# Kernel tuning notes

Measured on AMD Instinct MI355X. Metric: run time of the kernel, lower is better.

## Reference

```python
import jax, jax.numpy as jnp
import numpy as np

B, N, H = 16, 1024, 1024


def setup_inputs() -> dict:
    key = jax.random.key(0)
    ks = jax.random.split(key, 12)
    inv = 1.0 / np.sqrt(H)
    inp = {
        "x": jax.random.normal(ks[0], (B, N, H), jnp.float32),
        "atom_graph": jax.random.normal(ks[1], (B, N, N), jnp.float32),
        "variable_graph": jax.random.normal(ks[2], (B, N, N), jnp.float32),
        "Wq": jax.random.uniform(ks[3], (H, H), jnp.float32, -inv, inv),
        "bq": jax.random.uniform(ks[4], (H,), jnp.float32, -inv, inv),
        "Wk": jax.random.uniform(ks[5], (H, H), jnp.float32, -inv, inv),
        "bk": jax.random.uniform(ks[6], (H,), jnp.float32, -inv, inv),
        "Wv": jax.random.uniform(ks[7], (H, H), jnp.float32, -inv, inv),
        "bv": jax.random.uniform(ks[8], (H,), jnp.float32, -inv, inv),
        "predicate_pos": jax.random.randint(ks[9], (B, N), 0, 2, jnp.int32),
        "variable_tags": jax.random.randint(ks[10], (B, N), 0, 4, jnp.int32),
    }
    return inp


def _path_pool(h, predicate_pos):
    # h: [B,N,H]; predicate_pos: [B,N] in {0,1}
    b, n, d = h.shape
    i = jnp.arange(n)
    # pos[i-2] (value irrelevant for i<2, those branches handled explicitly)
    pp2 = jnp.pad(predicate_pos, ((0, 0), (2, 0)))[:, :n]  # [B,N]
    # window [s, e): i==0 -> [0,2); i==1 -> [0,3); pos[i-2]==1 -> [i,i+2); else [i-1,i+2)
    s = jnp.where(i < 2, 0, jnp.where(pp2 == 1, i, i - 1))  # [B,N]
    e = jnp.where(i == 0, 2, jnp.where(i == 1, 3, i + 2))    # [N]
    e = jnp.minimum(e, n)
    e = jnp.broadcast_to(e, (b, n))
    # prefix sums along node dim with a leading zero row -> windowed means via gather
    cs = jnp.concatenate([jnp.zeros((b, 1, d), h.dtype), jnp.cumsum(h, axis=1)], axis=1)  # [B,N+1,H]
    win_sum = (jnp.take_along_axis(cs, e[:, :, None], axis=1)
               - jnp.take_along_axis(cs, s[:, :, None], axis=1))  # [B,N,H]
    means = win_sum / (e - s)[:, :, None].astype(h.dtype)
    mask = (predicate_pos == 1).astype(h.dtype)  # [B,N]
    item = (means * mask[:, :, None]).sum(axis=1) / mask.sum(axis=1)[:, None]  # [B,H]
    return jnp.broadcast_to(item[:, None, :], (b, n, d))


def reference(x, atom_graph, variable_graph, Wq, bq, Wk, bk, Wv, bv,
              predicate_pos, variable_tags):
    scale = x.shape[-1] ** (-0.5)
    q = (x @ Wq.T + bq) * scale
    k = x @ Wk.T + bk
    v = x @ Wv.T + bv
    att = jnp.einsum("bnh,bmh->bnm", q, k) + atom_graph + variable_graph
    att = jax.nn.softmax(att, axis=-1)  # dropout is identity in eval
    h = jnp.einsum("bnm,bmh->bnh", att, v)
    return _path_pool(h, predicate_pos)
```

## Files before the change

kernel.cpp:

```cpp
#include <hip/hip_runtime.h>
#include <hip/hip_bf16.h>

#define BATCH 16
#define SEQ   1024
#define DIM   1024

typedef __attribute__((ext_vector_type(8))) short bf16x8;
typedef __attribute__((ext_vector_type(4))) float f32x4;
typedef __attribute__((ext_vector_type(4))) unsigned short us4;

__device__ __forceinline__ float bfu2f(unsigned short u) {
  union { unsigned int i; float f; } c; c.i = ((unsigned int)u) << 16; return c.f;
}
__device__ __forceinline__ unsigned short f2bfu(float f) {
  union { float f; unsigned int i; } c; c.f = f;
  return (unsigned short)((c.i + 0x7FFFu + ((c.i >> 16) & 1u)) >> 16);
}
__device__ __forceinline__ void async16(void* lds, const void* g) {
  __builtin_amdgcn_global_load_lds(
      (const __attribute__((address_space(1))) unsigned int*)g,
      (__attribute__((address_space(3))) unsigned int*)lds, 16, 0, 0);
}

__global__ void cast_xw_kernel(const float* __restrict__ x, const float* __restrict__ Wv,
                               unsigned short* __restrict__ xb,
                               unsigned short* __restrict__ Wvb, int x4) {
  int i = blockIdx.x * blockDim.x + threadIdx.x;
  const float* in; unsigned short* out; int j;
  if (i < x4) { in = x; out = xb; j = i; }
  else { in = Wv; out = Wvb; j = i - x4; }
  f32x4 v = ((const f32x4*)in)[j];
  us4 o;
  o[0] = f2bfu(v[0]); o[1] = f2bfu(v[1]); o[2] = f2bfu(v[2]); o[3] = f2bfu(v[3]);
  ((us4*)out)[j] = o;
}

__global__ void castT_kernel(const float* __restrict__ Wq, const float* __restrict__ Wk,
                             unsigned short* __restrict__ WqT,
                             unsigned short* __restrict__ WkT) {
  const float* in = (blockIdx.z == 0) ? Wq : Wk;
  unsigned short* out = (blockIdx.z == 0) ? WqT : WkT;
  __shared__ float t[64][65];
  const int h0 = blockIdx.x * 64, i0 = blockIdx.y * 64;
  const int tid = threadIdx.x;
  const int sub = tid >> 4, c4 = tid & 15;
#pragma unroll
  for (int p = 0; p < 4; ++p) {
    const int row = p * 16 + sub;
    f32x4 v = *(const f32x4*)(in + (size_t)(h0 + row) * DIM + i0 + c4 * 4);
    t[row][c4 * 4 + 0] = v[0]; t[row][c4 * 4 + 1] = v[1];
    t[row][c4 * 4 + 2] = v[2]; t[row][c4 * 4 + 3] = v[3];
  }
  __syncthreads();
#pragma unroll
  for (int p = 0; p < 4; ++p) {
    const int orow = p * 16 + sub;
    us4 o;
    o[0] = f2bfu(t[c4 * 4 + 0][orow]);
    o[1] = f2bfu(t[c4 * 4 + 1][orow]);
    o[2] = f2bfu(t[c4 * 4 + 2][orow]);
    o[3] = f2bfu(t[c4 * 4 + 3][orow]);
    *(us4*)(out + (size_t)(i0 + orow) * DIM + h0 + c4 * 4) = o;
  }
}

__global__ void t12_kernel(const unsigned short* __restrict__ WqT,
                           const unsigned short* __restrict__ WkT,
                           const float* __restrict__ bq, const float* __restrict__ bk,
                           float* __restrict__ t1, float* __restrict__ t2) {
  const int y = blockIdx.y;
  const unsigned short* Wt = y ? WkT : WqT;
  const float* vec = y ? bq : bk;
  float* tout = y ? t2 : t1;
  const int wave = threadIdx.x >> 6, lane = threadIdx.x & 63;
  const int i = blockIdx.x * 4 + wave;
  const us4* wr = (const us4*)(Wt + (size_t)i * DIM);
  float s = 0.f;
#pragma unroll
  for (int t = 0; t < 4; ++t) {
    us4 w4 = wr[lane + 64 * t];
    f32x4 b4 = *(const f32x4*)(vec + (lane + 64 * t) * 4);
    s += bfu2f(w4[0]) * b4[0] + bfu2f(w4[1]) * b4[1] +
         bfu2f(w4[2]) * b4[2] + bfu2f(w4[3]) * b4[3];
  }
#pragma unroll
  for (int o = 32; o; o >>= 1) s += __shfl_down(s, o);
  if (lane == 0) tout[i] = s;
}

__global__ void ac_kernel(const unsigned short* __restrict__ xb,
                          const float* __restrict__ t1, const float* __restrict__ t2,
                          const float* __restrict__ bq, const float* __restrict__ bk,
                          float* __restrict__ a, float* __restrict__ c) {
  const float scale = 0.03125f;
  const int tid = threadIdx.x;
  const int wave = tid >> 6, lane = tid & 63;
  float dp = 0.f;
  for (int i = tid; i < DIM; i += 256) dp += bq[i] * bk[i];
#pragma unroll
  for (int o = 32; o; o >>= 1) dp += __shfl_down(dp, o);
  __shared__ float dred[4];
  if ((tid & 63) == 0) dred[tid >> 6] = dp;
  __syncthreads();
  const float d = dred[0] + dred[1] + dred[2] + dred[3];
  float t1r[16], t2r[16];
#pragma unroll
  for (int t = 0; t < 4; ++t) {
    f32x4 v1 = *(const f32x4*)(t1 + (lane + 64 * t) * 4);
    f32x4 v2 = *(const f32x4*)(t2 + (lane + 64 * t) * 4);
#pragma unroll
    for (int j = 0; j < 4; ++j) { t1r[t * 4 + j] = v1[j]; t2r[t * 4 + j] = v2[j]; }
  }
  for (int rr = 0; rr < 16; ++rr) {
    const int row = blockIdx.x * 64 + wave * 16 + rr;
    const us4* xr = (const us4*)(xb + (size_t)row * DIM);
    float sa = 0.f, sc = 0.f;
#pragma unroll
    for (int t = 0; t < 4; ++t) {
      us4 v = xr[lane + 64 * t];
#pragma unroll
      for (int j = 0; j < 4; ++j) {
        const float f = bfu2f(v[j]);
        sa += f * t1r[t * 4 + j];
        sc += f * t2r[t * 4 + j];
      }
    }
#pragma unroll
    for (int o = 32; o; o >>= 1) { sa += __shfl_down(sa, o); sc += __shfl_down(sc, o); }
    if (lane == 0) {
      a[row] = scale * (sa + d);
      c[row] = scale * sc;
    }
  }
}

__global__ void pathw_kernel(const int* __restrict__ pos, float* __restrict__ w,
                             float* __restrict__ u, float* __restrict__ zbias) {
  const int b = blockIdx.x;
  __shared__ int ps[SEQ];
  __shared__ int mcnt;
  const int tid = threadIdx.x;
  if (tid == 0) mcnt = 0;
  __syncthreads();
  if (b == 0)
    for (int i = tid; i < DIM; i += 256) zbias[i] = 0.f;
  for (int i = tid; i < SEQ; i += 256) {
    ps[i] = pos[b * SEQ + i];
    u[b * SEQ + i] = 0.f;
  }
  __syncthreads();
  int c = 0;
  for (int i = tid; i < SEQ; i += 256) c += ps[i];
  for (int o = 32; o; o >>= 1) c += __shfl_down(c, o);
  if ((tid & 63) == 0) atomicAdd(&mcnt, c);
  __syncthreads();
  const float invM = 1.0f / (float)mcnt;
  for (int j = tid; j < SEQ; j += 256) {
    float a = 0.f;
#pragma unroll
    for (int di = -1; di <= 1; ++di) {
      int i = j + di;
      if (i < 0 || i >= SEQ) continue;
      if (!ps[i]) continue;
      int s, e;
      if (i < 2) { s = 0; e = (i == 0) ? 2 : 3; }
      else { s = (ps[i - 2] == 1) ? i : (i - 1); e = i + 2; if (e > SEQ) e = SEQ; }
      if (s <= j && j < e) a += 1.0f / (float)(e - s);
    }
    w[b * SEQ + j] = a * invM;
  }
}

__global__ void proj_gemm(const unsigned short* __restrict__ A,
                          const unsigned short* __restrict__ W,
                          const float* __restrict__ bias, float alpha,
                          unsigned short* __restrict__ C, int M, int N, int K)
{
  __shared__ __align__(16) char smem[32768];
  float* Sl = (float*)smem;
  const int tid = threadIdx.x;
  const int wave = tid >> 6, lane = tid & 63;
  const int lr = lane & 15, lg = lane >> 4;
  const int wr = wave >> 1, wc = wave & 1;
  const int flat = blockIdx.x + gridDim.x * blockIdx.y;
  const int q8 = (gridDim.x * gridDim.y) >> 3;
  const int t = (flat & 7) * q8 + (flat >> 3);
  const int m0 = (t / gridDim.y) * 128;
  const int n0 = (t % gridDim.y) * 128;
  const int off0 = tid * 16, off1 = 4096 + tid * 16;
  const int r0 = off0 >> 6, ke0 = (off0 >> 1) & 31;
  const int r1 = off1 >> 6, ke1 = (off1 >> 1) & 31;
  f32x4 acc[4][4] = {};

  auto stage = [&](char* base, int kk) {
    async16(base + off0, A + (size_t)(m0 + r0) * K + kk + ke0);
    async16(base + off1, A + (size_t)(m0 + r1) * K + kk + ke1);
    async16(base + 8192 + off0, W + (size_t)(n0 + r0) * K + kk + ke0);
    async16(base + 8192 + off1, W + (size_t)(n0 + r1) * K + kk + ke1);
  };
  auto compute = [&](const char* base) {
    bf16x8 af[4], bfv[4];
#pragma unroll
    for (int i = 0; i < 4; ++i) {
      af[i]  = *(const bf16x8*)(base + ((wr * 64 + i * 16 + lr) << 6) + (lg << 4));
      bfv[i] = *(const bf16x8*)(base + 8192 + ((wc * 64 + i * 16 + lr) << 6) + (lg << 4));
    }
#pragma unroll
    for (int i = 0; i < 4; ++i)
#pragma unroll
      for (int j = 0; j < 4; ++j)
        acc[i][j] = __builtin_amdgcn_mfma_f32_16x16x32_bf16(af[i], bfv[j], acc[i][j], 0, 0, 0);
  };

  const int nt = K >> 5;
  stage(smem, 0);
  __syncthreads();
  int cur = 0;
  for (int k = 0; k < nt - 1; ++k) {
    stage(smem + ((cur ^ 1) << 14), (k + 1) << 5);
    compute(smem + (cur << 14));
    __syncthreads();
    cur ^= 1;
  }
  compute(smem + (cur << 14));
#pragma unroll
  for (int p = 0; p < 4; ++p) {
    __syncthreads();
    if (wr == (p >> 1)) {
      const int ibase = (p & 1) * 2;
#pragma unroll
      for (int ii = 0; ii < 2; ++ii) {
        const int i = ibase + ii;
#pragma unroll
        for (int j = 0; j < 4; ++j)
#pragma unroll
          for (int r = 0; r < 4; ++r)
            Sl[(ii * 16 + lg * 4 + r) * 132 + wc * 64 + j * 16 + lr] = acc[i][j][r];
      }
    }
    __syncthreads();
#pragma unroll
    for (int it = 0; it < 4; ++it) {
      const int v = tid + it * 256;
      const int lrow = v >> 5, c4 = v & 31;
      const int grow = m0 + p * 32 + lrow;
      const int col = n0 + c4 * 4;
      const f32x4 s4 = *(const f32x4*)(&Sl[lrow * 132 + c4 * 4]);
      const f32x4 b4 = *(const f32x4*)(bias + col);
      us4 o;
      o[0] = f2bfu((s4[0] + b4[0]) * alpha);
      o[1] = f2bfu((s4[1] + b4[1]) * alpha);
      o[2] = f2bfu((s4[2] + b4[2]) * alpha);
      o[3] = f2bfu((s4[3] + b4[3]) * alpha);
      *(us4*)(C + (size_t)grow * N + col) = o;
    }
  }
}

__global__ void sgemm_kernel(const unsigned short* __restrict__ z,
                             const unsigned short* __restrict__ xb,
                             unsigned short* __restrict__ S)
{
  __shared__ __align__(16) char smem[33792];
  unsigned short* Slb = (unsigned short*)smem;
  const int flat = blockIdx.x + 8 * blockIdx.y + 64 * blockIdx.z;
  const int t = (flat & 7) * 128 + (flat >> 3);
  const int b = t >> 6;
  const int m0 = (t & 7) * 128;
  const int n0 = ((t >> 3) & 7) * 128;
  const unsigned short* Aq = z + ((size_t)b << 20);
  const unsigned short* Bk = xb + ((size_t)b << 20);
  const int tid = threadIdx.x;
  const int wave = tid >> 6, lane = tid & 63;
  const int lr = lane & 15, lg = lane >> 4;
  const int wr = wave >> 1, wc = wave & 1;
  const int off0 = tid * 16, off1 = 4096 + tid * 16;
  const int r0 = off0 >> 6, ke0 = (off0 >> 1) & 31;
  const int r1 = off1 >> 6, ke1 = (off1 >> 1) & 31;
  f32x4 acc[4][4] = {};

  auto stage = [&](char* base, int kk) {
    async16(base + off0, Aq + (size_t)(m0 + r0) * DIM + kk + ke0);
    async16(base + off1, Aq + (size_t)(m0 + r1) * DIM + kk + ke1);
    async16(base + 8192 + off0, Bk + (size_t)(n0 + r0) * DIM + kk + ke0);
    async16(base + 8192 + off1, Bk + (size_t)(n0 + r1) * DIM + kk + ke1);
  };
  auto compute = [&](const char* base) {
    bf16x8 af[4], bfv[4];
#pragma unroll
    for (int i = 0; i < 4; ++i) {
      af[i]  = *(const bf16x8*)(base + ((wr * 64 + i * 16 + lr) << 6) + (lg << 4));
      bfv[i] = *(const bf16x8*)(base + 8192 + ((wc * 64 + i * 16 + lr) << 6) + (lg << 4));
    }
#pragma unroll
    for (int i = 0; i < 4; ++i)
#pragma unroll
      for (int j = 0; j < 4; ++j)
        acc[i][j] = __builtin_amdgcn_mfma_f32_16x16x32_bf16(af[i], bfv[j], acc[i][j], 0, 0, 0);
  };

  stage(smem, 0);
  __syncthreads();
  int cur = 0;
  for (int k = 0; k < 31; ++k) {
    stage(smem + ((cur ^ 1) << 14), (k + 1) << 5);
    compute(smem + (cur << 14));
    __syncthreads();
    cur ^= 1;
  }
  compute(smem + (cur << 14));
  __syncthreads();
#pragma unroll
  for (int i = 0; i < 4; ++i)
#pragma unroll
    for (int j = 0; j < 4; ++j)
#pragma unroll
      for (int r = 0; r < 4; ++r)
        Slb[(wr * 64 + i * 16 + lg * 4 + r) * 132 + wc * 64 + j * 16 + lr] =
            f2bfu(acc[i][j][r]);
  __syncthreads();
  unsigned short* Sb = S + ((size_t)b << 20);
#pragma unroll
  for (int it = 0; it < 16; ++it) {
    const int v = tid + it * 256;
    const int lrow = v >> 5, c4 = v & 31;
    *(us4*)(Sb + (size_t)(m0 + lrow) * SEQ + n0 + c4 * 4) =
        *(const us4*)(&Slb[lrow * 132 + c4 * 4]);
  }
}

__global__ void exp_fused_kernel(const unsigned short* __restrict__ S,
                                 const float* __restrict__ ag, const float* __restrict__ vg,
                                 const float* __restrict__ av, const float* __restrict__ cv,
                                 const float* __restrict__ w, float* __restrict__ u)
{
  __shared__ float uacc[4][SEQ];
  const int b = blockIdx.y;
  const int tid = threadIdx.x;
  const int wave = tid >> 6, lane = tid & 63;
  for (int i = tid; i < 4 * SEQ; i += 256) ((float*)uacc)[i] = 0.f;
  __syncthreads();
  const float* agb = ag + ((size_t)b << 20);
  const float* vgb = vg + ((size_t)b << 20);
  const unsigned short* Sb = S + ((size_t)b << 20);
  const float* cvb = cv + b * SEQ;
  f32x4 cq[4];
#pragma unroll
  for (int qi = 0; qi < 4; ++qi)
    cq[qi] = *(const f32x4*)(cvb + (lane + 64 * qi) * 4);
  const int r0 = blockIdx.x * 8 + wave * 2;
#pragma unroll
  for (int r = 0; r < 2; ++r) {
    const int row = r0 + r;
    const float wrow = w[b * SEQ + row];
    if (wrow == 0.f) continue;
    const float arow = av[b * SEQ + row];
    us4 sv[4]; f32x4 a4[4], g4[4];
#pragma unroll
    for (int qi = 0; qi < 4; ++qi) {
      const size_t base = (size_t)row * SEQ + (lane + 64 * qi) * 4;
      sv[qi] = *(const us4*)(Sb + base);
      a4[qi] = *(const f32x4*)(agb + base);
      g4[qi] = *(const f32x4*)(vgb + base);
    }
    float e[16];
    float rs = 0.f;
#pragma unroll
    for (int qi = 0; qi < 4; ++qi)
#pragma unroll
      for (int j = 0; j < 4; ++j) {
        const float ev = __expf(bfu2f(sv[qi][j]) + a4[qi][j] + g4[qi][j] + arow + cq[qi][j]);
        e[qi * 4 + j] = ev;
        rs += ev;
      }
#pragma unroll
    for (int o2 = 32; o2; o2 >>= 1) rs += __shfl_xor(rs, o2);
    const float cn = wrow / rs;
#pragma unroll
    for (int qi = 0; qi < 4; ++qi) {
      const int col = (lane + 64 * qi) * 4;
#pragma unroll
      for (int j = 0; j < 4; ++j)
        uacc[wave][col + j] += cn * e[qi * 4 + j];
    }
  }
  __syncthreads();
  const int col = tid * 4;
  f32x4 s0 = *(const f32x4*)(&uacc[0][col]);
  const f32x4 s1 = *(const f32x4*)(&uacc[1][col]);
  const f32x4 s2 = *(const f32x4*)(&uacc[2][col]);
  const f32x4 s3 = *(const f32x4*)(&uacc[3][col]);
  s0[0] += s1[0] + s2[0] + s3[0];
  s0[1] += s1[1] + s2[1] + s3[1];
  s0[2] += s1[2] + s2[2] + s3[2];
  s0[3] += s1[3] + s2[3] + s3[3];
  float* ub = u + b * SEQ + col;
  atomicAdd(ub + 0, s0[0]);
  atomicAdd(ub + 1, s0[1]);
  atomicAdd(ub + 2, s0[2]);
  atomicAdd(ub + 3, s0[3]);
}

__global__ void wcol_kernel(const unsigned short* __restrict__ Mt,
                            const float* __restrict__ wv,
                            float* __restrict__ part) {
  const int nc = blockIdx.x;
  const int b = blockIdx.y;
  const int tid = threadIdx.x;
  __shared__ float c[64];
  if (tid < 64) c[tid] = wv[b * SEQ + nc * 64 + tid];
  __syncthreads();
  const unsigned short* p = Mt + ((size_t)b << 20) + ((size_t)(nc * 64) << 10) + tid * 4;
  f32x4 acc = {0.f, 0.f, 0.f, 0.f};
#pragma unroll 8
  for (int n = 0; n < 64; ++n) {
    const us4 v = *(const us4*)(p + ((size_t)n << 10));
    const float cn = c[n];
    acc[0] += cn * bfu2f(v[0]); acc[1] += cn * bfu2f(v[1]);
    acc[2] += cn * bfu2f(v[2]); acc[3] += cn * bfu2f(v[3]);
  }
  *(f32x4*)(part + (size_t)((b * 16 + nc) << 10) + tid * 4) = acc;
}

__global__ void wred_kernel(const float* __restrict__ part, float* __restrict__ vec) {
  const int b = blockIdx.x;
  const int tid = threadIdx.x;
  f32x4 s = {0.f, 0.f, 0.f, 0.f};
#pragma unroll
  for (int nc = 0; nc < 16; ++nc) {
    const f32x4 v = *(const f32x4*)(part + (size_t)((b * 16 + nc) << 10) + tid * 4);
    s[0] += v[0]; s[1] += v[1]; s[2] += v[2]; s[3] += v[3];
  }
  *(f32x4*)(vec + b * SEQ + tid * 4) = s;
}

__global__ void item_kernel(const float* __restrict__ y,
                            const unsigned short* __restrict__ Wvb,
                            const float* __restrict__ bv, float* __restrict__ item) {
  const int b = blockIdx.x;
  const int hblk = blockIdx.y;
  __shared__ float ys[DIM];
  const int tid = threadIdx.x;
  for (int i = tid; i < DIM; i += 256) ys[i] = y[b * DIM + i];
  __syncthreads();
  const int wave = tid >> 6, lane = tid & 63;
  const int h = hblk * 4 + wave;
  const us4* wrow = (const us4*)(Wvb + (size_t)h * DIM);
  float acc = 0.f;
#pragma unroll
  for (int t = 0; t < 4; ++t) {
    us4 v = wrow[t * 64 + lane];
    const int d0 = (t * 64 + lane) * 4;
    acc += ys[d0] * bfu2f(v[0]) + ys[d0 + 1] * bfu2f(v[1]) +
           ys[d0 + 2] * bfu2f(v[2]) + ys[d0 + 3] * bfu2f(v[3]);
  }
  for (int o = 32; o; o >>= 1) acc += __shfl_down(acc, o);
  if (lane == 0) item[b * DIM + h] = acc + bv[h];
}

__global__ void bcast_kernel(const float* __restrict__ item, float* __restrict__ out) {
  const int b = blockIdx.y;
  const int n = blockIdx.x;
  const f32x4* src = (const f32x4*)(item + b * DIM);
  f32x4* dst = (f32x4*)(out + (((size_t)b * SEQ + n) << 10));
  dst[threadIdx.x] = src[threadIdx.x];
}

extern "C" void kernel_launch(void* const* d_in, const int* in_sizes, int n_in,
                              void* d_out, int out_size, void* d_ws, size_t ws_size,
                              hipStream_t stream) {
  const float* x    = (const float*)d_in[0];
  const float* ag   = (const float*)d_in[1];
  const float* vgr  = (const float*)d_in[2];
  const float* Wq   = (const float*)d_in[3];
  const float* bq   = (const float*)d_in[4];
  const float* Wk   = (const float*)d_in[5];
  const float* bk   = (const float*)d_in[6];
  const float* Wv   = (const float*)d_in[7];
  const float* bv   = (const float*)d_in[8];
  const int*   pos  = (const int*)d_in[9];
  float* out = (float*)d_out;

  char* ws = (char*)d_ws;
  size_t off = 0;
  auto alloc = [&](size_t bytes) { void* p = ws + off; off += (bytes + 255) & ~(size_t)255; return p; };
  const size_t BNH = (size_t)BATCH * SEQ * DIM;
  unsigned short* xb   = (unsigned short*)alloc(BNH * 2);
  unsigned short* zb   = (unsigned short*)alloc(BNH * 2);
  unsigned short* S    = (unsigned short*)alloc(BNH * 2);
  unsigned short* WqT  = (unsigned short*)alloc((size_t)DIM * DIM * 2);
  unsigned short* WkT  = (unsigned short*)alloc((size_t)DIM * DIM * 2);
  unsigned short* Wvb  = (unsigned short*)alloc((size_t)DIM * DIM * 2);
  unsigned short* Hb   = (unsigned short*)alloc((size_t)DIM * DIM * 2);
  float* w     = (float*)alloc((size_t)BATCH * SEQ * 4);
  float* u     = (float*)alloc((size_t)BATCH * SEQ * 4);
  float* av    = (float*)alloc((size_t)BATCH * SEQ * 4);
  float* cvv   = (float*)alloc((size_t)BATCH * SEQ * 4);
  float* t1    = (float*)alloc((size_t)DIM * 4);
  float* t2    = (float*)alloc((size_t)DIM * 4);
  float* zbias = (float*)alloc((size_t)DIM * 4);
  float* y     = (float*)alloc((size_t)BATCH * DIM * 4);
  float* item  = (float*)alloc((size_t)BATCH * DIM * 4);
  float* part  = (float*)alloc((size_t)BATCH * 16 * SEQ * 4);

  const float scale = 0.03125f;
  const int x4 = (int)(BNH / 4);

  cast_xw_kernel<<<(x4 + DIM * DIM / 4) / 256, 256, 0, stream>>>(x, Wv, xb, Wvb, x4);
  castT_kernel<<<dim3(16, 16, 2), 256, 0, stream>>>(Wq, Wk, WqT, WkT);

  pathw_kernel<<<BATCH, 256, 0, stream>>>(pos, w, u, zbias);

  t12_kernel<<<dim3(256, 2), 256, 0, stream>>>(WqT, WkT, bq, bk, t1, t2);
  ac_kernel<<<256, 256, 0, stream>>>(xb, t1, t2, bq, bk, av, cvv);

  proj_gemm<<<dim3(8, 8), 256, 0, stream>>>(WkT, WqT, zbias, scale, Hb, DIM, DIM, DIM);

  proj_gemm<<<dim3(128, 8), 256, 0, stream>>>(xb, Hb, zbias, 1.0f, zb,
                                              BATCH * SEQ, DIM, DIM);

  sgemm_kernel<<<dim3(8, 8, BATCH), 256, 0, stream>>>(zb, xb, S);

  exp_fused_kernel<<<dim3(128, BATCH), 256, 0, stream>>>(S, ag, vgr, av, cvv, w, u);

  wcol_kernel<<<dim3(16, BATCH), 256, 0, stream>>>(xb, u, part);
  wred_kernel<<<BATCH, 256, 0, stream>>>(part, y);

  item_kernel<<<dim3(BATCH, 256), 256, 0, stream>>>(y, Wvb, bv, item);

  bcast_kernel<<<dim3(SEQ, BATCH), 256, 0, stream>>>(item, out);
}
```

Baseline: 237.3 us.

## Prefetch two GEMM stages ahead and replace softmax atomics with partial reduction

Both bf16 GEMM kernels now issue the loads for the first two k-tiles up front. In the main loop they wait with a partial vmcnt and raw s_barrier, so the next tile's global-to-LDS load overlaps the current tile's MFMA work and one sync per iteration goes away. The exp/softmax kernel now accumulates per-row contributions in registers and writes per-block partials, instead of doing LDS read-modify-write followed by global atomicAdd. A second wred pass reduces those partials, which drops the u zero-init but adds an extra launch and a larger partial buffer.

```diff
diff --git a/kernel.cpp b/kernel.cpp
--- a/kernel.cpp
+++ b/kernel.cpp
@@ -135,7 +135,7 @@
 }
 
 __global__ void pathw_kernel(const int* __restrict__ pos, float* __restrict__ w,
-                             float* __restrict__ u, float* __restrict__ zbias) {
+                             float* __restrict__ zbias) {
   const int b = blockIdx.x;
   __shared__ int ps[SEQ];
   __shared__ int mcnt;
@@ -144,10 +144,7 @@
   __syncthreads();
   if (b == 0)
     for (int i = tid; i < DIM; i += 256) zbias[i] = 0.f;
-  for (int i = tid; i < SEQ; i += 256) {
-    ps[i] = pos[b * SEQ + i];
-    u[b * SEQ + i] = 0.f;
-  }
+  for (int i = tid; i < SEQ; i += 256) ps[i] = pos[b * SEQ + i];
   __syncthreads();
   int c = 0;
   for (int i = tid; i < SEQ; i += 256) c += ps[i];
@@ -214,14 +211,18 @@
 
   const int nt = K >> 5;
   stage(smem, 0);
-  __syncthreads();
+  stage(smem + 16384, 32);
   int cur = 0;
   for (int k = 0; k < nt - 1; ++k) {
-    stage(smem + ((cur ^ 1) << 14), (k + 1) << 5);
+    asm volatile("s_waitcnt vmcnt(4)" ::: "memory");
+    __builtin_amdgcn_s_barrier();
     compute(smem + (cur << 14));
-    __syncthreads();
+    __builtin_amdgcn_s_barrier();
+    if (k + 2 < nt) stage(smem + (cur << 14), (k + 2) << 5);
     cur ^= 1;
   }
+  asm volatile("s_waitcnt vmcnt(0)" ::: "memory");
+  __builtin_amdgcn_s_barrier();
   compute(smem + (cur << 14));
 #pragma unroll
   for (int p = 0; p < 4; ++p) {
@@ -300,14 +301,18 @@
   };
 
   stage(smem, 0);
-  __syncthreads();
+  stage(smem + 16384, 32);
   int cur = 0;
   for (int k = 0; k < 31; ++k) {
-    stage(smem + ((cur ^ 1) << 14), (k + 1) << 5);
+    asm volatile("s_waitcnt vmcnt(4)" ::: "memory");
+    __builtin_amdgcn_s_barrier();
     compute(smem + (cur << 14));
-    __syncthreads();
+    __builtin_amdgcn_s_barrier();
+    if (k + 2 < 32) stage(smem + (cur << 14), (k + 2) << 5);
     cur ^= 1;
   }
+  asm volatile("s_waitcnt vmcnt(0)" ::: "memory");
+  __builtin_amdgcn_s_barrier();
   compute(smem + (cur << 14));
   __syncthreads();
 #pragma unroll
@@ -332,14 +337,12 @@
 __global__ void exp_fused_kernel(const unsigned short* __restrict__ S,
                                  const float* __restrict__ ag, const float* __restrict__ vg,
                                  const float* __restrict__ av, const float* __restrict__ cv,
-                                 const float* __restrict__ w, float* __restrict__ u)
+                                 const float* __restrict__ w, float* __restrict__ part)
 {
-  __shared__ float uacc[4][SEQ];
+  __shared__ float red[4][SEQ];
   const int b = blockIdx.y;
   const int tid = threadIdx.x;
   const int wave = tid >> 6, lane = tid & 63;
-  for (int i = tid; i < 4 * SEQ; i += 256) ((float*)uacc)[i] = 0.f;
-  __syncthreads();
   const float* agb = ag + ((size_t)b << 20);
   const float* vgb = vg + ((size_t)b << 20);
   const unsigned short* Sb = S + ((size_t)b << 20);
@@ -348,6 +351,7 @@
 #pragma unroll
   for (int qi = 0; qi < 4; ++qi)
     cq[qi] = *(const f32x4*)(cvb + (lane + 64 * qi) * 4);
+  f32x4 ur[4] = {};
   const int r0 = blockIdx.x * 8 + wave * 2;
 #pragma unroll
   for (int r = 0; r < 2; ++r) {
@@ -377,28 +381,25 @@
     for (int o2 = 32; o2; o2 >>= 1) rs += __shfl_xor(rs, o2);
     const float cn = wrow / rs;
 #pragma unroll
-    for (int qi = 0; qi < 4; ++qi) {
-      const int col = (lane + 64 * qi) * 4;
+    for (int qi = 0; qi < 4; ++qi)
 #pragma unroll
       for (int j = 0; j < 4; ++j)
-        uacc[wave][col + j] += cn * e[qi * 4 + j];
-    }
-  }
+        ur[qi][j] += cn * e[qi * 4 + j];
+  }
+#pragma unroll
+  for (int qi = 0; qi < 4; ++qi)
+    *(f32x4*)(&red[wave][(lane + 64 * qi) * 4]) = ur[qi];
   __syncthreads();
   const int col = tid * 4;
-  f32x4 s0 = *(const f32x4*)(&uacc[0][col]);
-  const f32x4 s1 = *(const f32x4*)(&uacc[1][col]);
-  const f32x4 s2 = *(const f32x4*)(&uacc[2][col]);
-  const f32x4 s3 = *(const f32x4*)(&uacc[3][col]);
+  f32x4 s0 = *(const f32x4*)(&red[0][col]);
+  const f32x4 s1 = *(const f32x4*)(&red[1][col]);
+  const f32x4 s2 = *(const f32x4*)(&red[2][col]);
+  const f32x4 s3 = *(const f32x4*)(&red[3][col]);
   s0[0] += s1[0] + s2[0] + s3[0];
   s0[1] += s1[1] + s2[1] + s3[1];
   s0[2] += s1[2] + s2[2] + s3[2];
   s0[3] += s1[3] + s2[3] + s3[3];
-  float* ub = u + b * SEQ + col;
-  atomicAdd(ub + 0, s0[0]);
-  atomicAdd(ub + 1, s0[1]);
-  atomicAdd(ub + 2, s0[2]);
-  atomicAdd(ub + 3, s0[3]);
+  *(f32x4*)(part + ((size_t)(b * 128 + blockIdx.x) << 10) + col) = s0;
 }
 
 __global__ void wcol_kernel(const unsigned short* __restrict__ Mt,
@@ -422,13 +423,13 @@
   *(f32x4*)(part + (size_t)((b * 16 + nc) << 10) + tid * 4) = acc;
 }
 
-__global__ void wred_kernel(const float* __restrict__ part, float* __restrict__ vec) {
+__global__ void wred_kernel(const float* __restrict__ part, float* __restrict__ vec,
+                            int nchunks) {
   const int b = blockIdx.x;
   const int tid = threadIdx.x;
   f32x4 s = {0.f, 0.f, 0.f, 0.f};
-#pragma unroll
-  for (int nc = 0; nc < 16; ++nc) {
-    const f32x4 v = *(const f32x4*)(part + (size_t)((b * 16 + nc) << 10) + tid * 4);
+  for (int nc = 0; nc < nchunks; ++nc) {
+    const f32x4 v = *(const f32x4*)(part + ((size_t)(b * nchunks + nc) << 10) + tid * 4);
     s[0] += v[0]; s[1] += v[1]; s[2] += v[2]; s[3] += v[3];
   }
   *(f32x4*)(vec + b * SEQ + tid * 4) = s;
@@ -501,7 +502,7 @@
   float* zbias = (float*)alloc((size_t)DIM * 4);
   float* y     = (float*)alloc((size_t)BATCH * DIM * 4);
   float* item  = (float*)alloc((size_t)BATCH * DIM * 4);
-  float* part  = (float*)alloc((size_t)BATCH * 16 * SEQ * 4);
+  float* part  = (float*)alloc((size_t)BATCH * 128 * SEQ * 4);
 
   const float scale = 0.03125f;
   const int x4 = (int)(BNH / 4);
@@ -509,7 +510,7 @@
   cast_xw_kernel<<<(x4 + DIM * DIM / 4) / 256, 256, 0, stream>>>(x, Wv, xb, Wvb, x4);
   castT_kernel<<<dim3(16, 16, 2), 256, 0, stream>>>(Wq, Wk, WqT, WkT);
 
-  pathw_kernel<<<BATCH, 256, 0, stream>>>(pos, w, u, zbias);
+  pathw_kernel<<<BATCH, 256, 0, stream>>>(pos, w, zbias);
 
   t12_kernel<<<dim3(256, 2), 256, 0, stream>>>(WqT, WkT, bq, bk, t1, t2);
   ac_kernel<<<256, 256, 0, stream>>>(xb, t1, t2, bq, bk, av, cvv);
@@ -521,10 +522,11 @@
 
   sgemm_kernel<<<dim3(8, 8, BATCH), 256, 0, stream>>>(zb, xb, S);
 
-  exp_fused_kernel<<<dim3(128, BATCH), 256, 0, stream>>>(S, ag, vgr, av, cvv, w, u);
+  exp_fused_kernel<<<dim3(128, BATCH), 256, 0, stream>>>(S, ag, vgr, av, cvv, w, part);
+  wred_kernel<<<BATCH, 256, 0, stream>>>(part, u, 128);
 
   wcol_kernel<<<dim3(16, BATCH), 256, 0, stream>>>(xb, u, part);
-  wred_kernel<<<BATCH, 256, 0, stream>>>(part, y);
+  wred_kernel<<<BATCH, 256, 0, stream>>>(part, y, 16);
 
   item_kernel<<<dim3(BATCH, 256), 256, 0, stream>>>(y, Wvb, bv, item);
 
```

Result: slower. 243.0 us (+2.4%).
